# Performance work log

Measured on AMD Instinct MI355X. Metric: run time of the kernel, lower is better.

Reference implementation:

```python
import jax, jax.numpy as jnp
import numpy as np
import itertools

# ---- static config (mirrors args in init_kwargs) ----
BS = 4                        # num_processes
H, W = 480, 640               # frame_height, frame_width
NC = 16                       # num_sem_categories
C = 4 + NC                    # obs channels: RGB + depth + semantics
RES = 5                       # map_resolution (cm per cell)
ZRES = 5
MAP_CM = 4800 // 2            # map_size_cm // global_downscaling
M = MAP_CM // RES             # 480 local-map cells
VR = 100                      # vision_range
FOV = 79.0                    # hfov (deg)
DU = 1                        # du_scale
AGENT_H = 1.55 * 100.0        # camera_height * 100 (cm)
MAXH = int(360 / ZRES)        # 72
MINH = int(-40 / ZRES)        # -8
ZH = MAXH - MINH              # 80 height bins
MAP_THR, EXP_THR, CAT_THR = 1.0, 1.0, 5.0
DEG = 57.29577951308232
MIN_Z = int(5 / ZRES - MINH)                    # 9
MAX_Z = int((AGENT_H + 1 + 50) / ZRES - MINH)   # 49
XCAM = (W - 1.0) / 2.0
ZCAM = (H - 1.0) / 2.0
FOC = (W / 2.0) / np.tan(np.deg2rad(FOV / 2.0))


def _splat_feat_nd(feat, coords, grid_dims):
    # feat: (B,F,N) ; coords: (B,3,N) normalized to [-1,1] ; trilinear scatter-add
    B, Fc, N = feat.shape
    G = grid_dims[0] * grid_dims[1] * grid_dims[2]
    grid_flat = jnp.zeros((B, Fc, G), feat.dtype)
    pos_dim, wts_dim = [], []
    for d in range(3):
        gd = grid_dims[d]
        pos = coords[:, d, :] * (gd / 2.0) + gd / 2.0   # (B,N) voxel-space coord
        fl = jnp.floor(pos)
        pd, wd = [], []
        for ix in (0.0, 1.0):
            pos_ix = fl + ix
            safe = ((pos_ix > 0) & (pos_ix < gd)).astype(feat.dtype)
            wd.append((1.0 - jnp.abs(pos - pos_ix)) * safe)
            pd.append(pos_ix * safe)  # unsafe points dumped at index 0 with weight 0
        pos_dim.append(pd)
        wts_dim.append(wd)
    for ix_d in itertools.product((0, 1), (0, 1), (0, 1)):
        w = wts_dim[0][ix_d[0]] * wts_dim[1][ix_d[1]] * wts_dim[2][ix_d[2]]
        idx = jnp.zeros_like(w)
        for d in range(3):
            idx = idx * grid_dims[d] + pos_dim[d][ix_d[d]]
        idx = idx.astype(jnp.int32)                     # (B,N)
        vals = feat * w[:, None, :]                     # (B,F,N)
        grid_flat = jax.vmap(lambda g, i, v: g.at[:, i].add(v))(grid_flat, idx, vals)
    grid_flat = jnp.round(grid_flat)
    return grid_flat.reshape((B, Fc) + tuple(grid_dims))


def _affine_grid(theta, Hh, Ww):
    # align_corners=True base grid
    xs = jnp.linspace(-1.0, 1.0, Ww)
    ys = jnp.linspace(-1.0, 1.0, Hh)
    Xg, Yg = jnp.meshgrid(xs, ys)
    base = jnp.stack([Xg, Yg, jnp.ones_like(Xg)], -1)   # (H,W,3)
    return jnp.einsum('bij,hwj->bhwi', theta, base)     # (B,H,W,2)


def _grid_sample(img, grid):
    # bilinear, align_corners=True, zero padding; img (B,C,H,W), grid (B,Ho,Wo,2)
    B, Cc, Hh, Ww = img.shape
    x = (grid[..., 0] + 1.0) * 0.5 * (Ww - 1)
    y = (grid[..., 1] + 1.0) * 0.5 * (Hh - 1)
    x0 = jnp.floor(x)
    y0 = jnp.floor(y)
    wx1 = x - x0
    wy1 = y - y0

    def gather(ix, iy):
        valid = ((ix >= 0) & (ix <= Ww - 1) & (iy >= 0) & (iy <= Hh - 1)).astype(img.dtype)
        ixc = jnp.clip(ix, 0, Ww - 1).astype(jnp.int32)
        iyc = jnp.clip(iy, 0, Hh - 1).astype(jnp.int32)
        v = jax.vmap(lambda im, yy, xx: im[:, yy, xx])(img, iyc, ixc)  # (B,C,Ho,Wo)
        return v * valid[:, None]

    return (gather(x0, y0) * ((1 - wx1) * (1 - wy1))[:, None]
            + gather(x0 + 1, y0) * (wx1 * (1 - wy1))[:, None]
            + gather(x0, y0 + 1) * ((1 - wx1) * wy1)[:, None]
            + gather(x0 + 1, y0 + 1) * (wx1 * wy1)[:, None])


def _forward(obs, pose_obs, maps_last, poses_last, view_angles):
    bs = obs.shape[0]
    depth = obs[:, 3, ::DU, ::DU]                        # (B,h,w) depth in cm
    gx = jnp.arange(W, dtype=obs.dtype)[None, None, ::DU]
    gz = jnp.arange(H - 1, -1, -1, dtype=obs.dtype)[None, ::DU, None]
    Xp = (gx - XCAM) * depth / FOC
    Zp = (gz - ZCAM) * depth / FOC
    # rotate about x-axis by per-env view angle (deg), then lift by agent height
    a = jnp.deg2rad(view_angles)[:, None, None]
    ca, sa = jnp.cos(a), jnp.sin(a)
    Xv = Xp
    Yv = ca * depth - sa * Zp
    Zv = sa * depth + ca * Zp + AGENT_H
    # shift_loc rotation angle is pi/2 - pi/2 = 0 -> identity rot, only x shift
    Xv = Xv + VR * RES / 2.0
    # normalize to [-1,1] voxel coords
    xs = (Xv / RES - VR // 2.0) / VR * 2.0
    ys = (Yv / RES - VR // 2.0) / VR * 2.0
    zs = (Zv / ZRES - (MAXH + MINH) // 2.0) / (MAXH - MINH) * 2.0
    coords = jnp.stack([xs, ys, zs], 1).reshape(bs, 3, -1)   # (B,3,N)
    # features: channel 0 = ones (occupancy), rest = avg-pooled semantic masks
    sem = obs[:, 4:]
    pooled = sem.reshape(bs, NC, H // DU, DU, W // DU, DU).mean((3, 5))
    N = (H // DU) * (W // DU)
    feat = jnp.concatenate([jnp.ones((bs, 1, N), obs.dtype), pooled.reshape(bs, NC, N)], 1)
    voxels = _splat_feat_nd(feat, coords, (VR, VR, ZH)).swapaxes(2, 3)  # (B,1+NC,VR,VR,ZH)
    agg = voxels[..., MIN_Z:MAX_Z].sum(4)
    fp_map_pred = jnp.clip(agg[:, :1] / MAP_THR, 0.0, 1.0)
    fp_exp_pred = jnp.clip(voxels.sum(4)[:, :1] / EXP_THR, 0.0, 1.0)
    cat_pred = jnp.clip(agg[:, 1:] / CAT_THR, 0.0, 1.0)
    agent_view = jnp.zeros((bs, C, M, M), obs.dtype)
    x1 = M // 2 - VR // 2
    x2 = x1 + VR
    y1 = M // 2
    y2 = y1 + VR
    agent_view = agent_view.at[:, 0:1, y1:y2, x1:x2].set(fp_map_pred)
    agent_view = agent_view.at[:, 1:2, y1:y2, x1:x2].set(fp_exp_pred)
    agent_view = agent_view.at[:, 4:, y1:y2, x1:x2].set(cat_pred)
    # pose integration (get_new_pose_batch, note sequential in-place semantics)
    o = poses_last[:, 2] / DEG
    yy = poses_last[:, 1] + pose_obs[:, 0] * jnp.sin(o) + pose_obs[:, 1] * jnp.cos(o)
    xx = poses_last[:, 0] + pose_obs[:, 0] * jnp.cos(o) - pose_obs[:, 1] * jnp.sin(o)
    tt = poses_last[:, 2] + pose_obs[:, 2] * DEG
    tt = jnp.fmod(tt - 180.0, 360.0) + 180.0
    tt = jnp.fmod(tt + 180.0, 360.0) - 180.0
    current_poses = jnp.stack([xx, yy, tt], 1)
    # st_pose is detached in the original
    st = jax.lax.stop_gradient(current_poses)
    half = M // 2
    stx = -(st[:, 0] * 100.0 / RES - half) / half
    sty = -(st[:, 1] * 100.0 / RES - half) / half
    t = (90.0 - st[:, 2]) * np.pi / 180.0
    ct, s_t = jnp.cos(t), jnp.sin(t)
    zero, one = jnp.zeros_like(ct), jnp.ones_like(ct)
    theta1 = jnp.stack([jnp.stack([ct, -s_t, zero], 1), jnp.stack([s_t, ct, zero], 1)], 1)
    theta2 = jnp.stack([jnp.stack([one, zero, stx], 1), jnp.stack([zero, one, sty], 1)], 1)
    rotated = _grid_sample(agent_view, _affine_grid(theta1, M, M))
    translated = _grid_sample(rotated, _affine_grid(theta2, M, M))
    map_pred = jnp.maximum(maps_last, translated)
    # pose_pred aliases the in-place-updated poses_last in torch == current_poses
    return fp_map_pred, map_pred, current_poses, current_poses, translated


def setup_inputs() -> dict:
    key = jax.random.key(0)
    k1, k2, k3, k4 = jax.random.split(key, 4)
    obs = jax.random.uniform(k1, (BS, C, H, W), jnp.float32)
    obs = obs.at[:, 3].multiply(400.0)  # depth channel in cm, up to 4 m
    pose_obs = jax.random.uniform(k2, (BS, 3), jnp.float32) * 0.25
    maps_last = jax.random.uniform(k3, (BS, C, M, M), jnp.float32)
    poses_last = jax.random.uniform(k4, (BS, 3), jnp.float32)
    view_angles = jnp.zeros((BS,), jnp.float32)
    return {"obs": obs, "pose_obs": pose_obs, "maps_last": maps_last,
            "poses_last": poses_last, "view_angles": view_angles}


def reference(obs, pose_obs, maps_last, poses_last, view_angles):
    return _forward(obs, pose_obs, maps_last, poses_last, view_angles)
```

## Files before the change

kernel.cpp:

```cpp
#include <hip/hip_runtime.h>
#include <math.h>

#define BS 4
#define HH 480
#define WW 640
#define NPX (HH * WW)
#define NC 16
#define CHN 20
#define MM 480
#define VRD 100
#define ZHD 80
#define MINZ 9
#define MAXZ 49
#define CAP 8192

#define OFF0 0
#define OFF1 40000
#define OFF2 18472000
#define OFF3 18472012
#define OFF4 18472024
#define OFFM 28840000
#define OFFC 36113600
#define OFFS 36120000
#define GEO  40000

__device__ __forceinline__ void pix2pos(int w, int h, float depth, float ca, float sa,
                                        float foc, float& px, float& py, float& pz) {
    float gx = (float)w;
    float gz = (float)(HH - 1 - h);
    float Xp = (gx - 319.5f) * depth / foc;
    float Zp = (gz - 239.5f) * depth / foc;
    float Yv = ca * depth - sa * Zp;
    float Zv = sa * depth + ca * Zp + 155.0f;
    float Xv = Xp + 250.0f;
    float xs = (Xv / 5.0f - 50.0f) / 100.0f * 2.0f;
    float ys = (Yv / 5.0f - 50.0f) / 100.0f * 2.0f;
    float zs = (Zv / 5.0f - 32.0f) / 80.0f * 2.0f;
    px = xs * 50.0f + 50.0f;
    py = ys * 50.0f + 50.0f;
    pz = zs * 40.0f + 40.0f;
}

__global__ __launch_bounds__(256) void bin_kernel(const float* __restrict__ obs,
                                                  const float* __restrict__ va,
                                                  int* __restrict__ cnt,
                                                  float4* __restrict__ geo,
                                                  float foc) {
    int idx = blockIdx.x * blockDim.x + threadIdx.x;
    if (idx >= BS * NPX) return;
    int b   = idx / NPX;
    int rem = idx % NPX;
    float depth = obs[((size_t)b * CHN + 3) * NPX + rem];
    int h = rem / WW, w = rem % WW;
    float a  = va[b] * 0.017453292519943295f;
    float ca = cosf(a), sa = sinf(a);
    float px, py, pz;
    pix2pos(w, h, depth, ca, sa, foc, px, py, pz);
    int f = (int)floorf(py);
    if (f < 0 || f > 99) return;
    int slot = atomicAdd(cnt + (b * VRD + f) * 16, 1);
    if (slot < CAP) {
        float4 r;
        r.x = px; r.y = py; r.z = pz; r.w = __int_as_float(rem);
        geo[(size_t)(b * VRD + f) * CAP + slot] = r;
    }
}

__global__ __launch_bounds__(256, 6) void slice_kernel(const float* __restrict__ obs,
                                                       const int* __restrict__ cnt,
                                                       const float4* __restrict__ geo,
                                                       float* __restrict__ maps,
                                                       float* __restrict__ stage) {
    __shared__ float acc[40 * VRD];
    int bid  = blockIdx.x;
    int wgid = (bid & 7) * 900 + (bid >> 3);
    int s  = wgid % VRD;
    int p  = wgid / VRD;
    int b  = p & 3;
    int c  = p >> 2;
    int tid = threadIdx.x;
    for (int i = tid; i < 40 * VRD; i += 256) acc[i] = 0.0f;
    __syncthreads();

    bool isocc = (c >= 16);
    float clo   = isocc ? ((c == 16) ? 1.0f : 40.0f) : 9.0f;
    float chi   = isocc ? ((c == 16) ? 40.0f : 80.0f) : 49.0f;
    int   zbase = isocc ? ((c == 16) ? 0 : 40) : 9;
    const float* sb = isocc ? (const float*)0 : obs + ((size_t)b * CHN + 4 + c) * NPX;

    int sm1 = (s > 0) ? s - 1 : 0;
    int n0 = (s > 0) ? min(cnt[(b * VRD + sm1) * 16], CAP) : 0;
    int n1 = min(cnt[(b * VRD + s) * 16], CAP);
    const float4* g0 = geo + (size_t)(b * VRD + sm1) * CAP;
    const float4* g1 = geo + (size_t)(b * VRD + s) * CAP;
    int N = (s == 0) ? 0 : n0 + n1;
    float fs = (float)s;

    for (int base = tid * 4; base < N; base += 1024) {
        float4 g[4];
        #pragma unroll
        for (int j = 0; j < 4; j++) {
            int t = base + j;
            g[j] = (t < N) ? ((t < n0) ? g0[t] : g1[t - n0])
                           : make_float4(0.0f, -10.0f, 0.0f, 0.0f);
        }
        bool act[4];
        #pragma unroll
        for (int j = 0; j < 4; j++) {
            float wy = 1.0f - fabsf(g[j].y - fs);
            bool ok = (wy > 0.0f);
            ok = ok && (g[j].z > clo - 1.0f) && (g[j].z < chi);
            float fx = floorf(g[j].x);
            ok = ok && (fx + 1.0f > 0.0f) && (fx < 100.0f);
            act[j] = ok;
        }
        float sv[4];
        #pragma unroll
        for (int j = 0; j < 4; j++)
            sv[j] = (!isocc && act[j]) ? sb[__float_as_int(g[j].w)] : 1.0f;
        #pragma unroll
        for (int j = 0; j < 4; j++) {
            if (!act[j]) continue;
            float px = g[j].x, pz = g[j].z;
            float wy = 1.0f - fabsf(g[j].y - fs);
            float fx = floorf(px), fz = floorf(pz);
            #pragma unroll
            for (int i2 = 0; i2 < 2; i2++) {
                float cxp = fx + (float)i2;
                if (!(cxp > 0.0f && cxp < 100.0f)) continue;
                float wxy = wy * (1.0f - fabsf(px - cxp));
                int xi = (int)cxp;
                #pragma unroll
                for (int k = 0; k < 2; k++) {
                    float czp = fz + (float)k;
                    if (czp < clo || czp >= chi) continue;
                    float w3 = wxy * (1.0f - fabsf(pz - czp));
                    if (w3 == 0.0f) continue;
                    atomicAdd(&acc[((int)czp - zbase) * VRD + xi], w3 * sv[j]);
                }
            }
        }
    }
    __syncthreads();

    if (!isocc) {
        for (int x = tid; x < VRD; x += 256) {
            float ssum = 0.0f;
            #pragma unroll 8
            for (int z = 0; z < 40; z++) ssum += rintf(acc[z * VRD + x]);
            maps[((size_t)(b * 18 + 2 + c) * VRD + s) * VRD + x] =
                fminf(fmaxf(ssum * 0.2f, 0.0f), 1.0f);
        }
    } else {
        int cell0 = (c == 16) ? 0 : 40;
        for (int x = tid; x < VRD; x += 256) {
            float s_all = 0.0f, s_agg = 0.0f;
            #pragma unroll 8
            for (int z = 0; z < 40; z++) {
                float r = rintf(acc[z * VRD + x]);
                s_all += r;
                int cell = cell0 + z;
                if (cell >= MINZ && cell < MAXZ) s_agg += r;
            }
            int o = (b * VRD + s) * VRD + x;
            atomicAdd(stage + o, s_all);
            atomicAdd(stage + 40000 + o, s_agg);
        }
    }
}

__global__ __launch_bounds__(256) void fixup_kernel(const float* __restrict__ stage,
                                                    float* __restrict__ maps,
                                                    float* __restrict__ out0) {
    int idx = blockIdx.x * blockDim.x + threadIdx.x;
    if (idx >= BS * VRD * VRD) return;
    int b = idx / (VRD * VRD);
    int r = idx % (VRD * VRD);
    float all = stage[idx];
    float agg = stage[40000 + idx];
    float fm = fminf(fmaxf(agg, 0.0f), 1.0f);
    float fe = fminf(fmaxf(all, 0.0f), 1.0f);
    maps[(size_t)(b * 18 + 0) * 10000 + r] = fm;
    maps[(size_t)(b * 18 + 1) * 10000 + r] = fe;
    out0[idx] = fm;
}

__device__ __forceinline__ void pose_params(const float* __restrict__ pose_obs,
                                            const float* __restrict__ poses_last,
                                            int b, float& ct, float& st,
                                            float& stx, float& sty) {
    const float DEG = 57.29577951308232f;
    float o  = poses_last[b*3+2] / DEG;
    float so = sinf(o), co = cosf(o);
    float yy = poses_last[b*3+1] + pose_obs[b*3+0]*so + pose_obs[b*3+1]*co;
    float xx = poses_last[b*3+0] + pose_obs[b*3+0]*co - pose_obs[b*3+1]*so;
    float tt = poses_last[b*3+2] + pose_obs[b*3+2]*DEG;
    tt = fmodf(tt - 180.0f, 360.0f) + 180.0f;
    tt = fmodf(tt + 180.0f, 360.0f) - 180.0f;
    stx = -((xx*100.0f/5.0f) - 240.0f) / 240.0f;
    sty = -((yy*100.0f/5.0f) - 240.0f) / 240.0f;
    float t = (90.0f - tt) * 0.017453292519943295f;
    ct = cosf(t); st = sinf(t);
}

__global__ __launch_bounds__(64) void pose_kernel(const float* __restrict__ pose_obs,
                                                  const float* __restrict__ poses_last,
                                                  float* __restrict__ out) {
    int b = threadIdx.x;
    if (b >= BS) return;
    const float DEG = 57.29577951308232f;
    float o  = poses_last[b*3+2] / DEG;
    float so = sinf(o), co = cosf(o);
    float yy = poses_last[b*3+1] + pose_obs[b*3+0]*so + pose_obs[b*3+1]*co;
    float xx = poses_last[b*3+0] + pose_obs[b*3+0]*co - pose_obs[b*3+1]*so;
    float tt = poses_last[b*3+2] + pose_obs[b*3+2]*DEG;
    tt = fmodf(tt - 180.0f, 360.0f) + 180.0f;
    tt = fmodf(tt + 180.0f, 360.0f) - 180.0f;
    out[OFF2 + b*3+0] = xx; out[OFF2 + b*3+1] = yy; out[OFF2 + b*3+2] = tt;
    out[OFF3 + b*3+0] = xx; out[OFF3 + b*3+1] = yy; out[OFF3 + b*3+2] = tt;
}

__global__ __launch_bounds__(256) void rotate_kernel(const float* __restrict__ maps,
                                                     const float* __restrict__ pose_obs,
                                                     const float* __restrict__ poses_last,
                                                     float* __restrict__ rot) {
    int idx = blockIdx.x * blockDim.x + threadIdx.x;
    if (idx >= BS * MM * MM) return;
    int b   = idx / (MM * MM);
    int rem = idx % (MM * MM);
    int y   = rem / MM;
    int x   = rem % MM;
    float ct, st, stx, sty;
    pose_params(pose_obs, poses_last, b, ct, st, stx, sty);
    float Xg = -1.0f + (float)x * (2.0f / 479.0f);
    float Yg = -1.0f + (float)y * (2.0f / 479.0f);
    float gx = ct * Xg - st * Yg;
    float gy = st * Xg + ct * Yg;
    float xf = (gx + 1.0f) * 0.5f * 479.0f;
    float yf = (gy + 1.0f) * 0.5f * 479.0f;
    float x0 = floorf(xf), y0 = floorf(yf);
    float fx = xf - x0, fy = yf - y0;
    float cw[4] = {(1.0f - fx) * (1.0f - fy), fx * (1.0f - fy),
                   (1.0f - fx) * fy,          fx * fy};
    float cx[4] = {x0, x0 + 1.0f, x0, x0 + 1.0f};
    float cy[4] = {y0, y0, y0 + 1.0f, y0 + 1.0f};
    float acc[18];
    #pragma unroll
    for (int m = 0; m < 18; m++) acc[m] = 0.0f;
    #pragma unroll
    for (int k = 0; k < 4; k++) {
        float fxk = cx[k], fyk = cy[k];
        if (!(fxk >= 0.0f && fxk <= 479.0f && fyk >= 0.0f && fyk <= 479.0f)) continue;
        int ix = (int)fxk, iy = (int)fyk;
        if (iy < 240 || iy >= 340 || ix < 190 || ix >= 290) continue;
        int mi = iy - 240, mj = ix - 190;
        float w = cw[k];
        const float* mp = maps + (size_t)b * 18 * VRD * VRD + mi * VRD + mj;
        #pragma unroll
        for (int m = 0; m < 18; m++) acc[m] += w * mp[(size_t)m * VRD * VRD];
    }
    size_t obase = ((size_t)b * CHN) * MM * MM + (size_t)y * MM + x;
    rot[obase + (size_t)0 * MM * MM] = acc[0];
    rot[obase + (size_t)1 * MM * MM] = acc[1];
    rot[obase + (size_t)2 * MM * MM] = 0.0f;
    rot[obase + (size_t)3 * MM * MM] = 0.0f;
    #pragma unroll
    for (int m = 2; m < 18; m++)
        rot[obase + (size_t)(m + 2) * MM * MM] = acc[m];
}

__global__ __launch_bounds__(256) void translate_kernel(const float* __restrict__ rot,
                                                        const float* __restrict__ pose_obs,
                                                        const float* __restrict__ poses_last,
                                                        float* __restrict__ tr) {
    int idx = blockIdx.x * blockDim.x + threadIdx.x;
    if (idx >= BS * MM * MM) return;
    int b   = idx / (MM * MM);
    int rem = idx % (MM * MM);
    int y   = rem / MM;
    int x   = rem % MM;
    float ct, st, stx, sty;
    pose_params(pose_obs, poses_last, b, ct, st, stx, sty);
    float Xg = -1.0f + (float)x * (2.0f / 479.0f);
    float Yg = -1.0f + (float)y * (2.0f / 479.0f);
    float xf = (Xg + stx + 1.0f) * 0.5f * 479.0f;
    float yf = (Yg + sty + 1.0f) * 0.5f * 479.0f;
    float x0 = floorf(xf), y0 = floorf(yf);
    float fx = xf - x0, fy = yf - y0;
    float cw[4] = {(1.0f - fx) * (1.0f - fy), fx * (1.0f - fy),
                   (1.0f - fx) * fy,          fx * fy};
    float cxs[4] = {x0, x0 + 1.0f, x0, x0 + 1.0f};
    float cys[4] = {y0, y0, y0 + 1.0f, y0 + 1.0f};
    bool vk[4]; int offk[4];
    #pragma unroll
    for (int k = 0; k < 4; k++) {
        vk[k] = (cxs[k] >= 0.0f && cxs[k] <= 479.0f && cys[k] >= 0.0f && cys[k] <= 479.0f);
        offk[k] = vk[k] ? ((int)cys[k] * MM + (int)cxs[k]) : 0;
    }
    #pragma unroll
    for (int c = 0; c < CHN; c++) {
        const float* rp = rot + ((size_t)b * CHN + c) * MM * MM;
        float v = 0.0f;
        #pragma unroll
        for (int k = 0; k < 4; k++)
            if (vk[k]) v += cw[k] * rp[offk[k]];
        tr[((size_t)b * CHN + c) * MM * MM + (size_t)y * MM + x] = v;
    }
}

__global__ __launch_bounds__(256) void max_kernel(const float* __restrict__ maps_last,
                                                  const float* __restrict__ tr,
                                                  float* __restrict__ mp) {
    int i = blockIdx.x * blockDim.x + threadIdx.x;
    int n4 = BS * CHN * MM * MM / 4;
    if (i >= n4) return;
    float4 a = ((const float4*)maps_last)[i];
    float4 t = ((const float4*)tr)[i];
    float4 r;
    r.x = fmaxf(a.x, t.x);
    r.y = fmaxf(a.y, t.y);
    r.z = fmaxf(a.z, t.z);
    r.w = fmaxf(a.w, t.w);
    ((float4*)mp)[i] = r;
}

extern "C" void kernel_launch(void* const* d_in, const int* in_sizes, int n_in,
                              void* d_out, int out_size, void* d_ws, size_t ws_size,
                              hipStream_t stream) {
    const float* obs         = (const float*)d_in[0];
    const float* pose_obs    = (const float*)d_in[1];
    const float* maps_last   = (const float*)d_in[2];
    const float* poses_last  = (const float*)d_in[3];
    const float* view_angles = (const float*)d_in[4];
    float* out = (float*)d_out;

    float*  maps  = out + OFFM;
    float4* geo   = (float4*)(out + GEO);
    int*    cnt   = (int*)(out + OFFC);
    float*  stage = out + OFFS;

    hipMemsetAsync(cnt, 0, (6400 + 80000) * sizeof(float), stream);

    const float foc = (float)(320.0 / tan(39.5 * M_PI / 180.0));

    int npix = BS * NPX;
    bin_kernel<<<(npix + 255) / 256, 256, 0, stream>>>(obs, view_angles, cnt, geo, foc);

    slice_kernel<<<dim3(VRD * BS * 18), 256, 0, stream>>>(obs, cnt, geo, maps, stage);

    fixup_kernel<<<(BS * VRD * VRD + 255) / 256, 256, 0, stream>>>(stage, maps, out + OFF0);

    pose_kernel<<<1, 64, 0, stream>>>(pose_obs, poses_last, out);

    int nmap = BS * MM * MM;
    rotate_kernel<<<(nmap + 255) / 256, 256, 0, stream>>>(maps, pose_obs, poses_last,
                                                          out + OFF1);
    translate_kernel<<<(nmap + 255) / 256, 256, 0, stream>>>(out + OFF1, pose_obs,
                                                             poses_last, out + OFF4);
    int n4 = BS * CHN * MM * MM / 4;
    max_kernel<<<(n4 + 255) / 256, 256, 0, stream>>>(maps_last, out + OFF4, out + OFF1);
}
```

Before: 1.237 ms.

## Store compact pixel records and recompute geometry in slice kernel

The binning kernel now writes 8-byte records (pixel index, depth) instead of 16-byte precomputed positions, and the slice kernel recomputes the 3D position with pix2pos. Record loads are now coalesced, with each thread striding by 256 rather than taking four consecutive entries. The block-to-work mapping is also reordered so that consecutive work groups share batch and channel, which may improve cache reuse of the record buckets and semantic channels. The aim is to cut global memory traffic for the intermediate buffer at the cost of extra ALU work per point, including an integer divide and modulo.

New measurement: 1.243 ms. Within noise of the previous version (+0.5%).

```diff
diff --git a/kernel.cpp b/kernel.cpp
--- a/kernel.cpp
+++ b/kernel.cpp
@@ -22,7 +22,7 @@
 #define OFFM 28840000
 #define OFFC 36113600
 #define OFFS 36120000
-#define GEO  40000
+#define RECOFF 40000
 
 __device__ __forceinline__ void pix2pos(int w, int h, float depth, float ca, float sa,
                                         float foc, float& px, float& py, float& pz) {
@@ -44,7 +44,7 @@
 __global__ __launch_bounds__(256) void bin_kernel(const float* __restrict__ obs,
                                                   const float* __restrict__ va,
                                                   int* __restrict__ cnt,
-                                                  float4* __restrict__ geo,
+                                                  float2* __restrict__ rec,
                                                   float foc) {
     int idx = blockIdx.x * blockDim.x + threadIdx.x;
     if (idx >= BS * NPX) return;
@@ -60,24 +60,25 @@
     if (f < 0 || f > 99) return;
     int slot = atomicAdd(cnt + (b * VRD + f) * 16, 1);
     if (slot < CAP) {
-        float4 r;
-        r.x = px; r.y = py; r.z = pz; r.w = __int_as_float(rem);
-        geo[(size_t)(b * VRD + f) * CAP + slot] = r;
+        float2 r; r.x = __int_as_float(rem); r.y = depth;
+        rec[(size_t)(b * VRD + f) * CAP + slot] = r;
     }
 }
 
 __global__ __launch_bounds__(256, 6) void slice_kernel(const float* __restrict__ obs,
                                                        const int* __restrict__ cnt,
-                                                       const float4* __restrict__ geo,
+                                                       const float2* __restrict__ rec,
+                                                       const float* __restrict__ va,
                                                        float* __restrict__ maps,
-                                                       float* __restrict__ stage) {
+                                                       float* __restrict__ stage,
+                                                       float foc) {
     __shared__ float acc[40 * VRD];
     int bid  = blockIdx.x;
     int wgid = (bid & 7) * 900 + (bid >> 3);
-    int s  = wgid % VRD;
-    int p  = wgid / VRD;
-    int b  = p & 3;
-    int c  = p >> 2;
+    int b  = wgid / 1800;
+    int r_ = wgid % 1800;
+    int c  = r_ / 100;
+    int s  = r_ % 100;
     int tid = threadIdx.x;
     for (int i = tid; i < 40 * VRD; i += 256) acc[i] = 0.0f;
     __syncthreads();
@@ -88,53 +89,58 @@
     int   zbase = isocc ? ((c == 16) ? 0 : 40) : 9;
     const float* sb = isocc ? (const float*)0 : obs + ((size_t)b * CHN + 4 + c) * NPX;
 
+    float a  = va[b] * 0.017453292519943295f;
+    float ca = cosf(a), sa = sinf(a);
     int sm1 = (s > 0) ? s - 1 : 0;
     int n0 = (s > 0) ? min(cnt[(b * VRD + sm1) * 16], CAP) : 0;
     int n1 = min(cnt[(b * VRD + s) * 16], CAP);
-    const float4* g0 = geo + (size_t)(b * VRD + sm1) * CAP;
-    const float4* g1 = geo + (size_t)(b * VRD + s) * CAP;
+    const float2* g0 = rec + (size_t)(b * VRD + sm1) * CAP;
+    const float2* g1 = rec + (size_t)(b * VRD + s) * CAP;
     int N = (s == 0) ? 0 : n0 + n1;
     float fs = (float)s;
 
-    for (int base = tid * 4; base < N; base += 1024) {
-        float4 g[4];
+    int nblk = (N + 1023) >> 10;
+    for (int blk = 0; blk < nblk; blk++) {
+        int base = (blk << 10) + tid;
+        float2 rv[4]; bool vld[4];
         #pragma unroll
         for (int j = 0; j < 4; j++) {
-            int t = base + j;
-            g[j] = (t < N) ? ((t < n0) ? g0[t] : g1[t - n0])
-                           : make_float4(0.0f, -10.0f, 0.0f, 0.0f);
-        }
-        bool act[4];
+            int t = base + (j << 8);
+            vld[j] = (t < N);
+            rv[j] = vld[j] ? ((t < n0) ? g0[t] : g1[t - n0]) : make_float2(0.0f, 0.0f);
+        }
+        int rm[4]; float px[4], py[4], pz[4]; bool act[4];
         #pragma unroll
         for (int j = 0; j < 4; j++) {
-            float wy = 1.0f - fabsf(g[j].y - fs);
-            bool ok = (wy > 0.0f);
-            ok = ok && (g[j].z > clo - 1.0f) && (g[j].z < chi);
-            float fx = floorf(g[j].x);
+            rm[j] = __float_as_int(rv[j].x);
+            pix2pos(rm[j] % WW, rm[j] / WW, rv[j].y, ca, sa, foc, px[j], py[j], pz[j]);
+            float wy = 1.0f - fabsf(py[j] - fs);
+            bool ok = vld[j] && (wy > 0.0f);
+            ok = ok && (pz[j] > clo - 1.0f) && (pz[j] < chi);
+            float fx = floorf(px[j]);
             ok = ok && (fx + 1.0f > 0.0f) && (fx < 100.0f);
             act[j] = ok;
         }
         float sv[4];
         #pragma unroll
         for (int j = 0; j < 4; j++)
-            sv[j] = (!isocc && act[j]) ? sb[__float_as_int(g[j].w)] : 1.0f;
+            sv[j] = (!isocc && act[j]) ? sb[rm[j]] : 1.0f;
         #pragma unroll
         for (int j = 0; j < 4; j++) {
             if (!act[j]) continue;
-            float px = g[j].x, pz = g[j].z;
-            float wy = 1.0f - fabsf(g[j].y - fs);
-            float fx = floorf(px), fz = floorf(pz);
+            float wy = 1.0f - fabsf(py[j] - fs);
+            float fx = floorf(px[j]), fz = floorf(pz[j]);
             #pragma unroll
             for (int i2 = 0; i2 < 2; i2++) {
                 float cxp = fx + (float)i2;
                 if (!(cxp > 0.0f && cxp < 100.0f)) continue;
-                float wxy = wy * (1.0f - fabsf(px - cxp));
+                float wxy = wy * (1.0f - fabsf(px[j] - cxp));
                 int xi = (int)cxp;
                 #pragma unroll
                 for (int k = 0; k < 2; k++) {
                     float czp = fz + (float)k;
                     if (czp < clo || czp >= chi) continue;
-                    float w3 = wxy * (1.0f - fabsf(pz - czp));
+                    float w3 = wxy * (1.0f - fabsf(pz[j] - czp));
                     if (w3 == 0.0f) continue;
                     atomicAdd(&acc[((int)czp - zbase) * VRD + xi], w3 * sv[j]);
                 }
@@ -335,7 +341,7 @@
     float* out = (float*)d_out;
 
     float*  maps  = out + OFFM;
-    float4* geo   = (float4*)(out + GEO);
+    float2* rec   = (float2*)(out + RECOFF);
     int*    cnt   = (int*)(out + OFFC);
     float*  stage = out + OFFS;
 
@@ -344,9 +350,10 @@
     const float foc = (float)(320.0 / tan(39.5 * M_PI / 180.0));
 
     int npix = BS * NPX;
-    bin_kernel<<<(npix + 255) / 256, 256, 0, stream>>>(obs, view_angles, cnt, geo, foc);
-
-    slice_kernel<<<dim3(VRD * BS * 18), 256, 0, stream>>>(obs, cnt, geo, maps, stage);
+    bin_kernel<<<(npix + 255) / 256, 256, 0, stream>>>(obs, view_angles, cnt, rec, foc);
+
+    slice_kernel<<<dim3(VRD * BS * 18), 256, 0, stream>>>(obs, cnt, rec, view_angles,
+                                                          maps, stage, foc);
 
     fixup_kernel<<<(BS * VRD * VRD + 255) / 256, 256, 0, stream>>>(stage, maps, out + OFF0);
 
```
